# Kernel optimization log

Hardware: AMD Instinct MI355X
Metric: run time of the kernel (lower is better)

## Reference

```python
import jax, jax.numpy as jnp
import numpy as np

SEQ = 8192      # sequence_size
EMB = 64        # embedSize
NCLS = 2        # numClasses
NLEAF = 8192    # leaves of a perfect binary tree (13 levels)


def setup_inputs() -> dict:
    key = jax.random.key(0)
    ks = jax.random.split(key, 7)
    s = 0.02  # small init scale so 13 stacked relu-linears stay numerically sane
    return {
        "leaf_seqs": jax.random.normal(ks[0], (NLEAF, SEQ), jnp.float32),
        "emb_W": jax.random.normal(ks[1], (EMB, SEQ), jnp.float32) * s,
        "emb_b": jax.random.normal(ks[2], (EMB,), jnp.float32) * s,
        "W_W": jax.random.normal(ks[3], (EMB, 2 * EMB), jnp.float32) * s,
        "W_b": jax.random.normal(ks[4], (EMB,), jnp.float32) * s,
        "proj_W": jax.random.normal(ks[5], (NCLS, EMB), jnp.float32) * s,
        "proj_b": jax.random.normal(ks[6], (NCLS,), jnp.float32) * s,
    }


def reference(leaf_seqs, emb_W, emb_b, W_W, W_b, proj_W, proj_b):
    # Leaves: relu(embedding(seq)) for every leaf, batched. [NLEAF, EMB]
    h = jax.nn.relu(jnp.einsum('ns,es->ne', leaf_seqs, emb_W) + emb_b)
    # Internal nodes: combine adjacent sibling pairs level by level
    # (left-to-right recursion over a perfect binary tree == adjacent pairing).
    depth = int(np.log2(NLEAF))  # 13 levels, static Python loop
    for _ in range(depth):
        pair = jnp.concatenate([h[0::2], h[1::2]], axis=1)  # [N/2, 2*EMB]
        h = jax.nn.relu(jnp.einsum('nc,ec->ne', pair, W_W) + W_b)
    # Root: projection logits, [1, NCLS] (forward() only emits the root).
    return jnp.einsum('ne,ce->nc', h, proj_W) + proj_b
```

## Files before the change

### kernel.cpp

```cpp
#include <hip/hip_runtime.h>

#define SEQ   8192
#define EMB   64
#define NLEAF 8192
#define KQ    2048
#define KT    64
#define NT    (KQ / KT)

typedef __attribute__((ext_vector_type(4))) float        f32x4;
typedef __attribute__((ext_vector_type(4))) unsigned int u32x4;

__device__ __forceinline__ unsigned rne_pair(float x, float y) {
    const unsigned ux = __float_as_uint(x), uy = __float_as_uint(y);
    const unsigned rx = (ux + 0x7fffu + ((ux >> 16) & 1u)) >> 16;
    const unsigned ry = (uy + 0x7fffu + ((uy >> 16) & 1u)) & 0xffff0000u;
    return rx | ry;
}

__device__ __forceinline__ void mfma16(f32x4& d, const u32x4 a, const u32x4 b) {
    asm("v_mfma_f32_16x16x32_bf16 %0, %1, %2, %0" : "+v"(d) : "v"(a), "v"(b));
}

__device__ __forceinline__ u32x4 frag_rne(const float* buf, int row, int kk) {
    const int c = kk >> 2;
    const int s = row & 7;
    const char* base = (const char*)buf + row * 256;
    const f32x4 v0 = *(const f32x4*)(base + 16 * (c ^ s));
    const f32x4 v1 = *(const f32x4*)(base + 16 * ((c + 1) ^ s));
    u32x4 h;
    h[0] = rne_pair(v0.x, v0.y);
    h[1] = rne_pair(v0.z, v0.w);
    h[2] = rne_pair(v1.x, v1.y);
    h[3] = rne_pair(v1.z, v1.w);
    return h;
}

#define GLDS16(gp, lp) \
    __builtin_amdgcn_global_load_lds( \
        (const __attribute__((address_space(1))) void*)(gp), \
        (__attribute__((address_space(3))) void*)(lp), 16, 0, 0)

__global__ __launch_bounds__(256) void k_cvtW(const float* __restrict__ W,
                                              unsigned* __restrict__ Wt)
{
    const int gid  = blockIdx.x * 256 + threadIdx.x;
    const int chsw = gid & 7;
    const int row  = (gid >> 3) & 63;
    const int t    = (gid >> 9) & 31;
    const int q    = gid >> 14;
    const int c    = chsw ^ (row & 7);
    const float* src = W + (size_t)row * SEQ + q * KQ + t * KT + c * 8;
    const f32x4 a = *(const f32x4*)(src);
    const f32x4 b = *(const f32x4*)(src + 4);
    u32x4 v;
    v[0] = rne_pair(a.x, a.y);
    v[1] = rne_pair(a.z, a.w);
    v[2] = rne_pair(b.x, b.y);
    v[3] = rne_pair(b.z, b.w);
    u32x4* dst = (u32x4*)(Wt + ((q * 32 + t) * 512 + row * 8 + chsw) * 4);
    *dst = v;
}

__global__ __launch_bounds__(256, 2) void k_gemm(
        const float* __restrict__ A, const char* __restrict__ Wt,
        float* __restrict__ P)
{
    __shared__ float sA[3][64 * 64];
    __shared__ char  sW[3][8192];

    const int tid  = threadIdx.x;
    const int lane = tid & 63;
    const int wid  = tid >> 6;

    const int g     = blockIdx.x >> 2;
    const int q     = blockIdx.x & 3;
    const int gl0   = g * 64;
    const int kbase = q * KQ;

    const int lr = lane >> 4;
    const int lc = lane & 15;

    const float* pA0;
    const float* pA1;
    const float* pA2;
    const float* pA3;
    {
        const int r0 = wid * 16 + 0 * 4 + lr;
        const int r1 = wid * 16 + 1 * 4 + lr;
        const int r2 = wid * 16 + 2 * 4 + lr;
        const int r3 = wid * 16 + 3 * 4 + lr;
        pA0 = A + (size_t)(gl0 + r0) * SEQ + kbase + (lc ^ (r0 & 7)) * 4;
        pA1 = A + (size_t)(gl0 + r1) * SEQ + kbase + (lc ^ (r1 & 7)) * 4;
        pA2 = A + (size_t)(gl0 + r2) * SEQ + kbase + (lc ^ (r2 & 7)) * 4;
        pA3 = A + (size_t)(gl0 + r3) * SEQ + kbase + (lc ^ (r3 & 7)) * 4;
    }
    const char* pW = Wt + (size_t)(q * 32) * 8192 + (2 * wid) * 1024 + lane * 16;

    const int fr = lane & 15;
    const int fq = lane >> 4;

    f32x4 acc0 = {0.f, 0.f, 0.f, 0.f};
    f32x4 acc1 = {0.f, 0.f, 0.f, 0.f};
    f32x4 acc2 = {0.f, 0.f, 0.f, 0.f};
    f32x4 acc3 = {0.f, 0.f, 0.f, 0.f};

#define STAGE(bi_) do { \
    char* wdst = (char*)&sW[bi_][0] + 2 * wid * 1024; \
    GLDS16(pW, wdst); \
    GLDS16(pW + 1024, wdst + 1024); \
    pW += 8192; \
    GLDS16(pA0, &sA[bi_][(wid * 16 + 0) * 64]); \
    GLDS16(pA1, &sA[bi_][(wid * 16 + 4) * 64]); \
    GLDS16(pA2, &sA[bi_][(wid * 16 + 8) * 64]); \
    GLDS16(pA3, &sA[bi_][(wid * 16 + 12) * 64]); \
    pA0 += KT; pA1 += KT; pA2 += KT; pA3 += KT; \
} while (0)

#define COMPUTE(bi_) do { \
    const float* bufA_ = &sA[bi_][0]; \
    const char*  bufW_ = &sW[bi_][0]; \
    _Pragma("unroll") \
    for (int k32 = 0; k32 < 2; ++k32) { \
        const u32x4 af = frag_rne(bufA_, wid * 16 + fr, k32 * 32 + fq * 8); \
        const int baddr = fr * 128 + 16 * ((k32 * 4 + fq) ^ (fr & 7)); \
        const u32x4 b0 = *(const u32x4*)(bufW_ + baddr); \
        const u32x4 b1 = *(const u32x4*)(bufW_ + 2048 + baddr); \
        const u32x4 b2 = *(const u32x4*)(bufW_ + 4096 + baddr); \
        const u32x4 b3 = *(const u32x4*)(bufW_ + 6144 + baddr); \
        mfma16(acc0, af, b0); \
        mfma16(acc1, af, b1); \
        mfma16(acc2, af, b2); \
        mfma16(acc3, af, b3); \
    } \
} while (0)

    STAGE(0);
    STAGE(1);

    int bcur = 0, bnxt = 1, bfut = 2;
    #pragma unroll 1
    for (int t = 0; t < NT; ++t) {
        if (t + 1 < NT) asm volatile("s_waitcnt vmcnt(6)" ::: "memory");
        else            asm volatile("s_waitcnt vmcnt(0)" ::: "memory");
        __builtin_amdgcn_s_barrier();
        __builtin_amdgcn_sched_barrier(0);
        if (t + 2 < NT) STAGE(bfut);
        COMPUTE(bcur);
        const int tmp = bcur; bcur = bnxt; bnxt = bfut; bfut = tmp;
    }

#undef STAGE
#undef COMPUTE

    float* Pq = P + (size_t)q * NLEAF * EMB;
    const int row0 = gl0 + wid * 16 + fq * 4;
    #pragma unroll
    for (int r = 0; r < 4; ++r) {
        Pq[(size_t)(row0 + r) * EMB +  0 + fr] = acc0[r];
        Pq[(size_t)(row0 + r) * EMB + 16 + fr] = acc1[r];
        Pq[(size_t)(row0 + r) * EMB + 32 + fr] = acc2[r];
        Pq[(size_t)(row0 + r) * EMB + 48 + fr] = acc3[r];
    }
}

__device__ __forceinline__ void load_WtV(f32x4 (*WtV)[64],
                                         const float* __restrict__ WW, int tid) {
    const int e  = tid & 63;
    const int jg = tid >> 6;
    #pragma unroll
    for (int u = 0; u < 8; ++u) {
        const int j = jg * 8 + u;
        WtV[j][e] = *(const f32x4*)&WW[e * 128 + 4 * j];
    }
}

__device__ __forceinline__ float hsum4(const f32x4 a) {
    return a.x + a.y + a.z + a.w;
}

__device__ __forceinline__ float* tree_levels(float* bufA, float* bufB,
        const f32x4 (*WtV)[64], float wb, int n0, int nlv, int tid)
{
    const int lane = tid & 63;
    const int wid  = tid >> 6;
    float* src = bufA;
    float* dst = bufB;
    int n = n0;
    for (int lvl = 0; lvl < nlv; ++lvl) {
        const int nodes = n >> 1;
        for (int base = wid * 4; base < nodes; base += 16) {
            const int cnt = (nodes - base < 4) ? (nodes - base) : 4;
            if (cnt == 4) {
                f32x4 ac0 = {0.f,0.f,0.f,0.f}, ac1 = ac0, ac2 = ac0, ac3 = ac0;
                const float* x0 = src + (2 * (base + 0)) * 68;
                const float* x1 = src + (2 * (base + 1)) * 68;
                const float* x2 = src + (2 * (base + 2)) * 68;
                const float* x3 = src + (2 * (base + 3)) * 68;
                #pragma unroll
                for (int j = 0; j < 32; ++j) {
                    const f32x4 w4 = WtV[j][lane];
                    const int off = (j < 16) ? (4 * j) : (68 + 4 * (j - 16));
                    ac0 += w4 * *(const f32x4*)(x0 + off);
                    ac1 += w4 * *(const f32x4*)(x1 + off);
                    ac2 += w4 * *(const f32x4*)(x2 + off);
                    ac3 += w4 * *(const f32x4*)(x3 + off);
                }
                dst[(base + 0) * 68 + lane] = fmaxf(wb + hsum4(ac0), 0.f);
                dst[(base + 1) * 68 + lane] = fmaxf(wb + hsum4(ac1), 0.f);
                dst[(base + 2) * 68 + lane] = fmaxf(wb + hsum4(ac2), 0.f);
                dst[(base + 3) * 68 + lane] = fmaxf(wb + hsum4(ac3), 0.f);
            } else {
                for (int u = 0; u < cnt; ++u) {
                    f32x4 ac = {0.f, 0.f, 0.f, 0.f};
                    const float* x = src + (2 * (base + u)) * 68;
                    #pragma unroll
                    for (int j = 0; j < 32; ++j) {
                        const f32x4 w4 = WtV[j][lane];
                        const int off = (j < 16) ? (4 * j) : (68 + 4 * (j - 16));
                        ac += w4 * *(const f32x4*)(x + off);
                    }
                    dst[(base + u) * 68 + lane] = fmaxf(wb + hsum4(ac), 0.f);
                }
            }
        }
        __syncthreads();
        float* tswp = src; src = dst; dst = tswp;
        n = nodes;
    }
    return src;
}

__global__ __launch_bounds__(256) void k_tree32(const float* __restrict__ P,
        const float* __restrict__ eb, const float* __restrict__ WW,
        const float* __restrict__ Wb, float* __restrict__ roots)
{
    __shared__ float hA[32][68];
    __shared__ float hB[16][68];
    __shared__ f32x4 WtV[32][64];
    const int tid = threadIdx.x;
    const int b   = blockIdx.x;
    load_WtV(WtV, WW, tid);
    {
        const int lf = tid >> 3;
        const int e0 = (tid & 7) * 8;
        const size_t base = (size_t)(b * 32 + lf) * EMB + e0;
        f32x4 s0 = *(const f32x4*)&P[base];
        f32x4 s1 = *(const f32x4*)&P[base + 4];
        s0 += *(const f32x4*)&P[(size_t)1 * NLEAF * EMB + base];
        s1 += *(const f32x4*)&P[(size_t)1 * NLEAF * EMB + base + 4];
        s0 += *(const f32x4*)&P[(size_t)2 * NLEAF * EMB + base];
        s1 += *(const f32x4*)&P[(size_t)2 * NLEAF * EMB + base + 4];
        s0 += *(const f32x4*)&P[(size_t)3 * NLEAF * EMB + base];
        s1 += *(const f32x4*)&P[(size_t)3 * NLEAF * EMB + base + 4];
        s0 += *(const f32x4*)&eb[e0];
        s1 += *(const f32x4*)&eb[e0 + 4];
        s0.x = fmaxf(s0.x, 0.f); s0.y = fmaxf(s0.y, 0.f);
        s0.z = fmaxf(s0.z, 0.f); s0.w = fmaxf(s0.w, 0.f);
        s1.x = fmaxf(s1.x, 0.f); s1.y = fmaxf(s1.y, 0.f);
        s1.z = fmaxf(s1.z, 0.f); s1.w = fmaxf(s1.w, 0.f);
        *(f32x4*)&hA[lf][e0]     = s0;
        *(f32x4*)&hA[lf][e0 + 4] = s1;
    }
    const float wb = Wb[tid & 63];
    __syncthreads();
    float* root = tree_levels(&hA[0][0], &hB[0][0], WtV, wb, 32, 5, tid);
    if (tid < 64) roots[b * 64 + tid] = root[tid];
}

__global__ __launch_bounds__(256) void k_tail(const float* __restrict__ in,
        const float* __restrict__ WW, const float* __restrict__ Wb,
        const float* __restrict__ pW, const float* __restrict__ pb,
        float* __restrict__ l9, unsigned* __restrict__ cnt,
        float* __restrict__ out)
{
    __shared__ float hA[32][68];
    __shared__ float hB[16][68];
    __shared__ f32x4 WtV[32][64];
    __shared__ int sflag;
    const int tid = threadIdx.x;
    load_WtV(WtV, WW, tid);
    {
        const int r  = tid >> 4;
        const int e0 = (tid & 15) * 4;
        *(f32x4*)&hA[r][e0] =
            *(const f32x4*)&in[(size_t)(blockIdx.x * 16 + r) * EMB + e0];
    }
    const float wb = Wb[tid & 63];
    __syncthreads();
    float* root = tree_levels(&hA[0][0], &hB[0][0], WtV, wb, 16, 4, tid);
    if (tid < 64)
        __hip_atomic_store(&l9[blockIdx.x * 64 + tid], root[tid],
                           __ATOMIC_RELAXED, __HIP_MEMORY_SCOPE_AGENT);
    __threadfence();
    if (tid == 0)
        sflag = (__hip_atomic_fetch_add(cnt, 1u, __ATOMIC_ACQ_REL,
                                        __HIP_MEMORY_SCOPE_AGENT) == 15u);
    __syncthreads();
    if (!sflag) return;

    __builtin_amdgcn_fence(__ATOMIC_ACQUIRE, "agent");
    {
        const int r  = tid >> 4;
        const int e0 = (tid & 15) * 4;
        f32x4 v;
        v.x = __hip_atomic_load(&l9[r * 64 + e0 + 0], __ATOMIC_RELAXED, __HIP_MEMORY_SCOPE_AGENT);
        v.y = __hip_atomic_load(&l9[r * 64 + e0 + 1], __ATOMIC_RELAXED, __HIP_MEMORY_SCOPE_AGENT);
        v.z = __hip_atomic_load(&l9[r * 64 + e0 + 2], __ATOMIC_RELAXED, __HIP_MEMORY_SCOPE_AGENT);
        v.w = __hip_atomic_load(&l9[r * 64 + e0 + 3], __ATOMIC_RELAXED, __HIP_MEMORY_SCOPE_AGENT);
        *(f32x4*)&hA[r][e0] = v;
    }
    __syncthreads();
    root = tree_levels(&hA[0][0], &hB[0][0], WtV, wb, 16, 4, tid);
    if (tid < 64) {
        const float hv = root[tid];
        float t0 = hv * pW[tid];
        float t1 = hv * pW[64 + tid];
        #pragma unroll
        for (int off = 32; off > 0; off >>= 1) {
            t0 += __shfl_down(t0, off);
            t1 += __shfl_down(t1, off);
        }
        if (tid == 0) { out[0] = t0 + pb[0]; out[1] = t1 + pb[1]; }
    }
}

extern "C" void kernel_launch(void* const* d_in, const int* in_sizes, int n_in,
                              void* d_out, int out_size, void* d_ws, size_t ws_size,
                              hipStream_t stream)
{
    const float* A  = (const float*)d_in[0];
    const float* eW = (const float*)d_in[1];
    const float* eb = (const float*)d_in[2];
    const float* WW = (const float*)d_in[3];
    const float* Wb = (const float*)d_in[4];
    const float* pW = (const float*)d_in[5];
    const float* pb = (const float*)d_in[6];
    float* out = (float*)d_out;

    float*    P     = (float*)d_ws;
    float*    roots = P + (size_t)4 * NLEAF * EMB;
    float*    l9    = roots + 256 * EMB;
    unsigned* cnt   = (unsigned*)((char*)d_ws + 8 * 1024 * 1024 + 72 * 1024);
    char*     Wtil  = (char*)d_ws + (size_t)16 * 1024 * 1024;

    hipMemsetAsync(cnt, 0, 64, stream);
    k_cvtW  <<<dim3(256), dim3(256), 0, stream>>>(eW, (unsigned*)Wtil);
    k_gemm  <<<dim3(512), dim3(256), 0, stream>>>(A, Wtil, P);
    k_tree32<<<dim3(256), dim3(256), 0, stream>>>(P, eb, WW, Wb, roots);
    k_tail  <<<dim3(16),  dim3(256), 0, stream>>>(roots, WW, Wb, pW, pb,
                                                  l9, cnt, out);
}
```

Before: 85.73 us.

## Drop split-K in leaf GEMM, fuse bias+relu epilogue, fold counter reset into cvtW

The leaf embedding GEMM no longer splits K four ways. Each 512-thread block now computes 32 full rows over the whole K range with 256-wide K tiles and double buffering, then applies bias and relu before writing h directly. This removes the 4x partial-sum write and read and the reduction in the tree kernel. The hipMemsetAsync of the counter is replaced by an atomic store inside the conversion kernel. In exchange there are fewer blocks (256), each does more serial work, and the loop now needs an extra barrier per iteration.

Result: slower. 108.6 us (+26.6%).

```diff
diff --git a/kernel.cpp b/kernel.cpp
--- a/kernel.cpp
+++ b/kernel.cpp
@@ -3,9 +3,8 @@
 #define SEQ   8192
 #define EMB   64
 #define NLEAF 8192
-#define KQ    2048
-#define KT    64
-#define NT    (KQ / KT)
+#define KT    256
+#define NT    (SEQ / KT)
 
 typedef __attribute__((ext_vector_type(4))) float        f32x4;
 typedef __attribute__((ext_vector_type(4))) unsigned int u32x4;
@@ -21,10 +20,10 @@
     asm("v_mfma_f32_16x16x32_bf16 %0, %1, %2, %0" : "+v"(d) : "v"(a), "v"(b));
 }
 
-__device__ __forceinline__ u32x4 frag_rne(const float* buf, int row, int kk) {
+__device__ __forceinline__ u32x4 frag_rneA(const float* buf, int row, int kk) {
     const int c = kk >> 2;
     const int s = row & 7;
-    const char* base = (const char*)buf + row * 256;
+    const char* base = (const char*)buf + row * 1024;
     const f32x4 v0 = *(const f32x4*)(base + 16 * (c ^ s));
     const f32x4 v1 = *(const f32x4*)(base + 16 * ((c + 1) ^ s));
     u32x4 h;
@@ -41,15 +40,16 @@
         (__attribute__((address_space(3))) void*)(lp), 16, 0, 0)
 
 __global__ __launch_bounds__(256) void k_cvtW(const float* __restrict__ W,
-                                              unsigned* __restrict__ Wt)
-{
-    const int gid  = blockIdx.x * 256 + threadIdx.x;
-    const int chsw = gid & 7;
-    const int row  = (gid >> 3) & 63;
-    const int t    = (gid >> 9) & 31;
-    const int q    = gid >> 14;
-    const int c    = chsw ^ (row & 7);
-    const float* src = W + (size_t)row * SEQ + q * KQ + t * KT + c * 8;
+                                              unsigned* __restrict__ Wimg,
+                                              unsigned* __restrict__ cnt)
+{
+    const int gid = blockIdx.x * 256 + threadIdx.x;
+    if (gid == 0)
+        __hip_atomic_store(cnt, 0u, __ATOMIC_RELAXED, __HIP_MEMORY_SCOPE_AGENT);
+    const int s = gid & 31;
+    const int r = (gid >> 5) & 63;
+    const int t = gid >> 11;
+    const float* src = W + (size_t)r * SEQ + t * KT + 8 * (s ^ (r & 7));
     const f32x4 a = *(const f32x4*)(src);
     const f32x4 b = *(const f32x4*)(src + 4);
     u32x4 v;
@@ -57,110 +57,88 @@
     v[1] = rne_pair(a.z, a.w);
     v[2] = rne_pair(b.x, b.y);
     v[3] = rne_pair(b.z, b.w);
-    u32x4* dst = (u32x4*)(Wt + ((q * 32 + t) * 512 + row * 8 + chsw) * 4);
-    *dst = v;
-}
-
-__global__ __launch_bounds__(256, 2) void k_gemm(
-        const float* __restrict__ A, const char* __restrict__ Wt,
-        float* __restrict__ P)
-{
-    __shared__ float sA[3][64 * 64];
-    __shared__ char  sW[3][8192];
+    *(u32x4*)(Wimg + (size_t)gid * 4) = v;
+}
+
+__global__ __launch_bounds__(512, 2) void k_gemm(
+        const float* __restrict__ A, const char* __restrict__ Wimg,
+        const float* __restrict__ eb, float* __restrict__ h)
+{
+    __shared__ float sA[2][32 * 256];
+    __shared__ char  sW[2][32768];
 
     const int tid  = threadIdx.x;
     const int lane = tid & 63;
     const int wid  = tid >> 6;
-
-    const int g     = blockIdx.x >> 2;
-    const int q     = blockIdx.x & 3;
-    const int gl0   = g * 64;
-    const int kbase = q * KQ;
-
-    const int lr = lane >> 4;
-    const int lc = lane & 15;
-
-    const float* pA0;
-    const float* pA1;
-    const float* pA2;
-    const float* pA3;
-    {
-        const int r0 = wid * 16 + 0 * 4 + lr;
-        const int r1 = wid * 16 + 1 * 4 + lr;
-        const int r2 = wid * 16 + 2 * 4 + lr;
-        const int r3 = wid * 16 + 3 * 4 + lr;
-        pA0 = A + (size_t)(gl0 + r0) * SEQ + kbase + (lc ^ (r0 & 7)) * 4;
-        pA1 = A + (size_t)(gl0 + r1) * SEQ + kbase + (lc ^ (r1 & 7)) * 4;
-        pA2 = A + (size_t)(gl0 + r2) * SEQ + kbase + (lc ^ (r2 & 7)) * 4;
-        pA3 = A + (size_t)(gl0 + r3) * SEQ + kbase + (lc ^ (r3 & 7)) * 4;
-    }
-    const char* pW = Wt + (size_t)(q * 32) * 8192 + (2 * wid) * 1024 + lane * 16;
+    const int b    = blockIdx.x;
+    const int gl0  = b * 32;
+
+    const int ra = 4 * wid;
+    const float* pA0 = A + (size_t)(gl0 + ra + 0) * SEQ + (lane ^ ((ra + 0) & 7)) * 4;
+    const float* pA1 = A + (size_t)(gl0 + ra + 1) * SEQ + (lane ^ ((ra + 1) & 7)) * 4;
+    const float* pA2 = A + (size_t)(gl0 + ra + 2) * SEQ + (lane ^ ((ra + 2) & 7)) * 4;
+    const float* pA3 = A + (size_t)(gl0 + ra + 3) * SEQ + (lane ^ ((ra + 3) & 7)) * 4;
+    const char* pW0 = Wimg + (8 * wid + 0) * 512 + lane * 16;
+    const char* pW1 = Wimg + (8 * wid + 2) * 512 + lane * 16;
+    const char* pW2 = Wimg + (8 * wid + 4) * 512 + lane * 16;
+    const char* pW3 = Wimg + (8 * wid + 6) * 512 + lane * 16;
 
     const int fr = lane & 15;
     const int fq = lane >> 4;
-
-    f32x4 acc0 = {0.f, 0.f, 0.f, 0.f};
-    f32x4 acc1 = {0.f, 0.f, 0.f, 0.f};
-    f32x4 acc2 = {0.f, 0.f, 0.f, 0.f};
-    f32x4 acc3 = {0.f, 0.f, 0.f, 0.f};
+    const int mr = (wid & 1) * 16;
+    const int nc = (wid >> 1) * 16;
+    const int wrow = nc + fr;
+    const int wswz = wrow & 7;
+
+    f32x4 acc = {0.f, 0.f, 0.f, 0.f};
 
 #define STAGE(bi_) do { \
-    char* wdst = (char*)&sW[bi_][0] + 2 * wid * 1024; \
-    GLDS16(pW, wdst); \
-    GLDS16(pW + 1024, wdst + 1024); \
-    pW += 8192; \
-    GLDS16(pA0, &sA[bi_][(wid * 16 + 0) * 64]); \
-    GLDS16(pA1, &sA[bi_][(wid * 16 + 4) * 64]); \
-    GLDS16(pA2, &sA[bi_][(wid * 16 + 8) * 64]); \
-    GLDS16(pA3, &sA[bi_][(wid * 16 + 12) * 64]); \
-    pA0 += KT; pA1 += KT; pA2 += KT; pA3 += KT; \
+    GLDS16(pA0, &sA[bi_][(ra + 0) * 256]);  pA0 += KT; \
+    GLDS16(pA1, &sA[bi_][(ra + 1) * 256]);  pA1 += KT; \
+    GLDS16(pA2, &sA[bi_][(ra + 2) * 256]);  pA2 += KT; \
+    GLDS16(pA3, &sA[bi_][(ra + 3) * 256]);  pA3 += KT; \
+    GLDS16(pW0, &sW[bi_][(8 * wid + 0) * 512]);  pW0 += 32768; \
+    GLDS16(pW1, &sW[bi_][(8 * wid + 2) * 512]);  pW1 += 32768; \
+    GLDS16(pW2, &sW[bi_][(8 * wid + 4) * 512]);  pW2 += 32768; \
+    GLDS16(pW3, &sW[bi_][(8 * wid + 6) * 512]);  pW3 += 32768; \
 } while (0)
 
 #define COMPUTE(bi_) do { \
     const float* bufA_ = &sA[bi_][0]; \
     const char*  bufW_ = &sW[bi_][0]; \
     _Pragma("unroll") \
-    for (int k32 = 0; k32 < 2; ++k32) { \
-        const u32x4 af = frag_rne(bufA_, wid * 16 + fr, k32 * 32 + fq * 8); \
-        const int baddr = fr * 128 + 16 * ((k32 * 4 + fq) ^ (fr & 7)); \
-        const u32x4 b0 = *(const u32x4*)(bufW_ + baddr); \
-        const u32x4 b1 = *(const u32x4*)(bufW_ + 2048 + baddr); \
-        const u32x4 b2 = *(const u32x4*)(bufW_ + 4096 + baddr); \
-        const u32x4 b3 = *(const u32x4*)(bufW_ + 6144 + baddr); \
-        mfma16(acc0, af, b0); \
-        mfma16(acc1, af, b1); \
-        mfma16(acc2, af, b2); \
-        mfma16(acc3, af, b3); \
+    for (int k32 = 0; k32 < 8; ++k32) { \
+        const u32x4 af = frag_rneA(bufA_, mr + fr, k32 * 32 + fq * 8); \
+        const u32x4 bf = *(const u32x4*)(bufW_ + wrow * 512 \
+                                         + 16 * ((k32 * 4 + fq) ^ wswz)); \
+        mfma16(acc, af, bf); \
     } \
 } while (0)
 
     STAGE(0);
     STAGE(1);
 
-    int bcur = 0, bnxt = 1, bfut = 2;
     #pragma unroll 1
     for (int t = 0; t < NT; ++t) {
-        if (t + 1 < NT) asm volatile("s_waitcnt vmcnt(6)" ::: "memory");
+        if (t + 1 < NT) asm volatile("s_waitcnt vmcnt(8)" ::: "memory");
         else            asm volatile("s_waitcnt vmcnt(0)" ::: "memory");
         __builtin_amdgcn_s_barrier();
         __builtin_amdgcn_sched_barrier(0);
-        if (t + 2 < NT) STAGE(bfut);
-        COMPUTE(bcur);
-        const int tmp = bcur; bcur = bnxt; bnxt = bfut; bfut = tmp;
+        COMPUTE(t & 1);
+        asm volatile("s_waitcnt lgkmcnt(0)" ::: "memory");
+        __builtin_amdgcn_s_barrier();
+        __builtin_amdgcn_sched_barrier(0);
+        if (t + 2 < NT) STAGE(t & 1);
     }
 
 #undef STAGE
 #undef COMPUTE
 
-    float* Pq = P + (size_t)q * NLEAF * EMB;
-    const int row0 = gl0 + wid * 16 + fq * 4;
+    const float bias = eb[nc + fr];
     #pragma unroll
-    for (int r = 0; r < 4; ++r) {
-        Pq[(size_t)(row0 + r) * EMB +  0 + fr] = acc0[r];
-        Pq[(size_t)(row0 + r) * EMB + 16 + fr] = acc1[r];
-        Pq[(size_t)(row0 + r) * EMB + 32 + fr] = acc2[r];
-        Pq[(size_t)(row0 + r) * EMB + 48 + fr] = acc3[r];
-    }
+    for (int r = 0; r < 4; ++r)
+        h[(size_t)(gl0 + mr + fq * 4 + r) * EMB + nc + fr] =
+            fmaxf(acc[r] + bias, 0.0f);
 }
 
 __device__ __forceinline__ void load_WtV(f32x4 (*WtV)[64],
@@ -230,9 +208,9 @@
     return src;
 }
 
-__global__ __launch_bounds__(256) void k_tree32(const float* __restrict__ P,
-        const float* __restrict__ eb, const float* __restrict__ WW,
-        const float* __restrict__ Wb, float* __restrict__ roots)
+__global__ __launch_bounds__(256) void k_tree32(const float* __restrict__ h,
+        const float* __restrict__ WW, const float* __restrict__ Wb,
+        float* __restrict__ roots)
 {
     __shared__ float hA[32][68];
     __shared__ float hB[16][68];
@@ -244,22 +222,8 @@
         const int lf = tid >> 3;
         const int e0 = (tid & 7) * 8;
         const size_t base = (size_t)(b * 32 + lf) * EMB + e0;
-        f32x4 s0 = *(const f32x4*)&P[base];
-        f32x4 s1 = *(const f32x4*)&P[base + 4];
-        s0 += *(const f32x4*)&P[(size_t)1 * NLEAF * EMB + base];
-        s1 += *(const f32x4*)&P[(size_t)1 * NLEAF * EMB + base + 4];
-        s0 += *(const f32x4*)&P[(size_t)2 * NLEAF * EMB + base];
-        s1 += *(const f32x4*)&P[(size_t)2 * NLEAF * EMB + base + 4];
-        s0 += *(const f32x4*)&P[(size_t)3 * NLEAF * EMB + base];
-        s1 += *(const f32x4*)&P[(size_t)3 * NLEAF * EMB + base + 4];
-        s0 += *(const f32x4*)&eb[e0];
-        s1 += *(const f32x4*)&eb[e0 + 4];
-        s0.x = fmaxf(s0.x, 0.f); s0.y = fmaxf(s0.y, 0.f);
-        s0.z = fmaxf(s0.z, 0.f); s0.w = fmaxf(s0.w, 0.f);
-        s1.x = fmaxf(s1.x, 0.f); s1.y = fmaxf(s1.y, 0.f);
-        s1.z = fmaxf(s1.z, 0.f); s1.w = fmaxf(s1.w, 0.f);
-        *(f32x4*)&hA[lf][e0]     = s0;
-        *(f32x4*)&hA[lf][e0 + 4] = s1;
+        *(f32x4*)&hA[lf][e0]     = *(const f32x4*)&h[base];
+        *(f32x4*)&hA[lf][e0 + 4] = *(const f32x4*)&h[base + 4];
     }
     const float wb = Wb[tid & 63];
     __syncthreads();
@@ -337,16 +301,15 @@
     const float* pb = (const float*)d_in[6];
     float* out = (float*)d_out;
 
-    float*    P     = (float*)d_ws;
-    float*    roots = P + (size_t)4 * NLEAF * EMB;
+    float*    h     = (float*)d_ws;
+    float*    roots = h + (size_t)NLEAF * EMB;
     float*    l9    = roots + 256 * EMB;
-    unsigned* cnt   = (unsigned*)((char*)d_ws + 8 * 1024 * 1024 + 72 * 1024);
-    char*     Wtil  = (char*)d_ws + (size_t)16 * 1024 * 1024;
-
-    hipMemsetAsync(cnt, 0, 64, stream);
-    k_cvtW  <<<dim3(256), dim3(256), 0, stream>>>(eW, (unsigned*)Wtil);
-    k_gemm  <<<dim3(512), dim3(256), 0, stream>>>(A, Wtil, P);
-    k_tree32<<<dim3(256), dim3(256), 0, stream>>>(P, eb, WW, Wb, roots);
+    unsigned* cnt   = (unsigned*)(l9 + 16 * EMB);
+    char*     Wimg  = (char*)d_ws + (size_t)4 * 1024 * 1024;
+
+    k_cvtW  <<<dim3(256), dim3(256), 0, stream>>>(eW, (unsigned*)Wimg, cnt);
+    k_gemm  <<<dim3(256), dim3(512), 0, stream>>>(A, Wimg, eb, h);
+    k_tree32<<<dim3(256), dim3(256), 0, stream>>>(h, WW, Wb, roots);
     k_tail  <<<dim3(16),  dim3(256), 0, stream>>>(roots, WW, Wb, pW, pb,
                                                   l9, cnt, out);
 }
```

## Fuse tree tail into leaf-tree kernel via last-block reduction and drop memset

Applied to the files above, without the earlier changes.

Removes the separate tail kernel and the memset. The counter is now reset inside the weight-conversion kernel, and the last of the 256 tree blocks to finish does the remaining 8 levels on all 256 roots. The first of those levels is a hand-unrolled 4-node-per-wave combine, followed by tree_levels over 128 nodes. This saves two launches and a global round trip, but the final 8 levels now run serially on one block and shared memory per block grows a lot (about 64KB sroots plus larger hA/hB), which may lower occupancy for every block.

After: 147.4 us. 1.72x slower.

```diff
diff --git a/kernel.cpp b/kernel.cpp
--- a/kernel.cpp
+++ b/kernel.cpp
@@ -41,9 +41,12 @@
         (__attribute__((address_space(3))) void*)(lp), 16, 0, 0)
 
 __global__ __launch_bounds__(256) void k_cvtW(const float* __restrict__ W,
-                                              unsigned* __restrict__ Wt)
+                                              unsigned* __restrict__ Wt,
+                                              unsigned* __restrict__ cnt)
 {
     const int gid  = blockIdx.x * 256 + threadIdx.x;
+    if (gid == 0)
+        __hip_atomic_store(cnt, 0u, __ATOMIC_RELAXED, __HIP_MEMORY_SCOPE_AGENT);
     const int chsw = gid & 7;
     const int row  = (gid >> 3) & 63;
     const int t    = (gid >> 9) & 31;
@@ -230,16 +233,23 @@
     return src;
 }
 
-__global__ __launch_bounds__(256) void k_tree32(const float* __restrict__ P,
+__global__ __launch_bounds__(256) void k_tree(const float* __restrict__ P,
         const float* __restrict__ eb, const float* __restrict__ WW,
-        const float* __restrict__ Wb, float* __restrict__ roots)
-{
-    __shared__ float hA[32][68];
-    __shared__ float hB[16][68];
+        const float* __restrict__ Wb, const float* __restrict__ pW,
+        const float* __restrict__ pb, float* __restrict__ roots,
+        unsigned* __restrict__ cnt, float* __restrict__ out)
+{
+    __shared__ float hA[128][68];
+    __shared__ float hB[64][68];
     __shared__ f32x4 WtV[32][64];
-    const int tid = threadIdx.x;
-    const int b   = blockIdx.x;
+    __shared__ float sroots[256][64];
+    __shared__ int sflag;
+
+    const int tid  = threadIdx.x;
+    const int lane = tid & 63;
+    const int b    = blockIdx.x;
     load_WtV(WtV, WW, tid);
+
     {
         const int lf = tid >> 3;
         const int e0 = (tid & 7) * 8;
@@ -261,56 +271,52 @@
         *(f32x4*)&hA[lf][e0]     = s0;
         *(f32x4*)&hA[lf][e0 + 4] = s1;
     }
-    const float wb = Wb[tid & 63];
+    const float wb = Wb[lane];
     __syncthreads();
+
     float* root = tree_levels(&hA[0][0], &hB[0][0], WtV, wb, 32, 5, tid);
-    if (tid < 64) roots[b * 64 + tid] = root[tid];
-}
-
-__global__ __launch_bounds__(256) void k_tail(const float* __restrict__ in,
-        const float* __restrict__ WW, const float* __restrict__ Wb,
-        const float* __restrict__ pW, const float* __restrict__ pb,
-        float* __restrict__ l9, unsigned* __restrict__ cnt,
-        float* __restrict__ out)
-{
-    __shared__ float hA[32][68];
-    __shared__ float hB[16][68];
-    __shared__ f32x4 WtV[32][64];
-    __shared__ int sflag;
-    const int tid = threadIdx.x;
-    load_WtV(WtV, WW, tid);
-    {
-        const int r  = tid >> 4;
-        const int e0 = (tid & 15) * 4;
-        *(f32x4*)&hA[r][e0] =
-            *(const f32x4*)&in[(size_t)(blockIdx.x * 16 + r) * EMB + e0];
-    }
-    const float wb = Wb[tid & 63];
-    __syncthreads();
-    float* root = tree_levels(&hA[0][0], &hB[0][0], WtV, wb, 16, 4, tid);
     if (tid < 64)
-        __hip_atomic_store(&l9[blockIdx.x * 64 + tid], root[tid],
+        __hip_atomic_store(&roots[b * 64 + tid], root[tid],
                            __ATOMIC_RELAXED, __HIP_MEMORY_SCOPE_AGENT);
     __threadfence();
     if (tid == 0)
         sflag = (__hip_atomic_fetch_add(cnt, 1u, __ATOMIC_ACQ_REL,
-                                        __HIP_MEMORY_SCOPE_AGENT) == 15u);
+                                        __HIP_MEMORY_SCOPE_AGENT) == 255u);
     __syncthreads();
     if (!sflag) return;
 
     __builtin_amdgcn_fence(__ATOMIC_ACQUIRE, "agent");
+    for (int i = tid; i < 256 * 64; i += 256)
+        (&sroots[0][0])[i] = __hip_atomic_load(&roots[i], __ATOMIC_RELAXED,
+                                               __HIP_MEMORY_SCOPE_AGENT);
+    __syncthreads();
+
     {
-        const int r  = tid >> 4;
-        const int e0 = (tid & 15) * 4;
-        f32x4 v;
-        v.x = __hip_atomic_load(&l9[r * 64 + e0 + 0], __ATOMIC_RELAXED, __HIP_MEMORY_SCOPE_AGENT);
-        v.y = __hip_atomic_load(&l9[r * 64 + e0 + 1], __ATOMIC_RELAXED, __HIP_MEMORY_SCOPE_AGENT);
-        v.z = __hip_atomic_load(&l9[r * 64 + e0 + 2], __ATOMIC_RELAXED, __HIP_MEMORY_SCOPE_AGENT);
-        v.w = __hip_atomic_load(&l9[r * 64 + e0 + 3], __ATOMIC_RELAXED, __HIP_MEMORY_SCOPE_AGENT);
-        *(f32x4*)&hA[r][e0] = v;
+        const int wid = tid >> 6;
+        for (int base = wid * 4; base < 128; base += 16) {
+            f32x4 ac0 = {0.f,0.f,0.f,0.f}, ac1 = ac0, ac2 = ac0, ac3 = ac0;
+            const float* y0 = &sroots[2 * (base + 0)][0];
+            const float* y1 = &sroots[2 * (base + 1)][0];
+            const float* y2 = &sroots[2 * (base + 2)][0];
+            const float* y3 = &sroots[2 * (base + 3)][0];
+            #pragma unroll
+            for (int j = 0; j < 32; ++j) {
+                const f32x4 w4 = WtV[j][lane];
+                const int off = (j < 16) ? (4 * j) : (64 + 4 * (j - 16));
+                ac0 += w4 * *(const f32x4*)(y0 + off);
+                ac1 += w4 * *(const f32x4*)(y1 + off);
+                ac2 += w4 * *(const f32x4*)(y2 + off);
+                ac3 += w4 * *(const f32x4*)(y3 + off);
+            }
+            hA[base + 0][lane] = fmaxf(wb + hsum4(ac0), 0.f);
+            hA[base + 1][lane] = fmaxf(wb + hsum4(ac1), 0.f);
+            hA[base + 2][lane] = fmaxf(wb + hsum4(ac2), 0.f);
+            hA[base + 3][lane] = fmaxf(wb + hsum4(ac3), 0.f);
+        }
     }
     __syncthreads();
-    root = tree_levels(&hA[0][0], &hB[0][0], WtV, wb, 16, 4, tid);
+
+    root = tree_levels(&hA[0][0], &hB[0][0], WtV, wb, 128, 7, tid);
     if (tid < 64) {
         const float hv = root[tid];
         float t0 = hv * pW[tid];
@@ -339,14 +345,11 @@
 
     float*    P     = (float*)d_ws;
     float*    roots = P + (size_t)4 * NLEAF * EMB;
-    float*    l9    = roots + 256 * EMB;
-    unsigned* cnt   = (unsigned*)((char*)d_ws + 8 * 1024 * 1024 + 72 * 1024);
+    unsigned* cnt   = (unsigned*)(roots + 256 * EMB);
     char*     Wtil  = (char*)d_ws + (size_t)16 * 1024 * 1024;
 
-    hipMemsetAsync(cnt, 0, 64, stream);
-    k_cvtW  <<<dim3(256), dim3(256), 0, stream>>>(eW, (unsigned*)Wtil);
-    k_gemm  <<<dim3(512), dim3(256), 0, stream>>>(A, Wtil, P);
-    k_tree32<<<dim3(256), dim3(256), 0, stream>>>(P, eb, WW, Wb, roots);
-    k_tail  <<<dim3(16),  dim3(256), 0, stream>>>(roots, WW, Wb, pW, pb,
-                                                  l9, cnt, out);
-}
+    k_cvtW<<<dim3(256), dim3(256), 0, stream>>>(eW, (unsigned*)Wtil, cnt);
+    k_gemm<<<dim3(512), dim3(256), 0, stream>>>(A, Wtil, P);
+    k_tree<<<dim3(256), dim3(256), 0, stream>>>(P, eb, WW, Wb, pW, pb,
+                                                roots, cnt, out);
+}
```
